# Kernel optimization log

Hardware: AMD Instinct MI355X
Metric: run time of the kernel (lower is better)

The kernel has to match this reference:

```python
import jax, jax.numpy as jnp
import numpy as np

N_QUBITS = 4
NOISE_RATE = 0.01  # depolarizing channel scales Pauli-Z expectation by (1 - p)


def _rx_mat(theta):
    # RX(theta) = [[cos(t/2), -i sin(t/2)], [-i sin(t/2), cos(t/2)]]; theta scalar or (b,)
    c = jnp.cos(theta / 2).astype(jnp.complex64)
    s = (-1j * jnp.sin(theta / 2)).astype(jnp.complex64)
    return jnp.stack([jnp.stack([c, s], -1), jnp.stack([s, c], -1)], -2)


def _apply_1q(state, mat, wire):
    # state: (b, 2,2,2,2); mat: (2,2) shared or (b,2,2) per-sample
    st = jnp.moveaxis(state, wire + 1, -1)
    if mat.ndim == 2:
        st = st @ mat.T
    else:
        st = jnp.einsum('b...j,bij->b...i', st, mat)
    return jnp.moveaxis(st, -1, wire + 1)


def _cnot(state, src, tgt):
    st = jnp.moveaxis(state, (src + 1, tgt + 1), (-2, -1))
    st = jnp.concatenate([st[..., 0:1, :], st[..., 1:2, ::-1]], axis=-2)
    return jnp.moveaxis(st, (-2, -1), (src + 1, tgt + 1))


def _qlayer(x, theta):
    # x: (b, n_qubits) encoding angles; theta: (n_params,) trainable RX angles
    b = x.shape[0]
    state = jnp.zeros((b,) + (2,) * N_QUBITS, jnp.complex64)
    state = state.at[(slice(None),) + (0,) * N_QUBITS].set(1.0)
    for w in range(N_QUBITS):                      # GeneralEncoder: RX(x_w) on wire w
        state = _apply_1q(state, _rx_mat(x[:, w]), w)
    for k in range(theta.shape[0]):                # trainable RX_k on wire k
        state = _apply_1q(state, _rx_mat(theta[k]), k)
    for i in range(N_QUBITS):                      # CNOT ring (i, (i+1)%n)
        state = _cnot(state, i, (i + 1) % N_QUBITS)
    p = jnp.abs(state) ** 2                        # (b, 2,2,2,2)
    ez = []
    for w in range(N_QUBITS):                      # <Z_w> = P(0) - P(1)
        axes = tuple(a for a in range(1, N_QUBITS + 1) if a != w + 1)
        m = p.sum(axes)
        ez.append(m[:, 0] - m[:, 1])
    return (1.0 - NOISE_RATE) * jnp.stack(ez, -1)  # depolarizing noise on expectations


def reference(inputs, w_lin, b_lin, w_map, b_map, theta):
    # inputs: (S, B, D); gate order: forget, input, update, output
    S, B, D = inputs.shape
    H = w_map.shape[1]
    hx0 = jnp.zeros((B, H), inputs.dtype)
    cx0 = jnp.zeros((B, H), inputs.dtype)
    qbatch = jax.vmap(_qlayer)  # over the 4 gates

    def step(carry, x):
        hx, cx = carry
        comb = jnp.concatenate([x, hx], axis=1)                      # (B, D+H)
        pre = jnp.einsum('gqd,bd->gbq', w_lin, comb) + b_lin[:, None, :]
        q = qbatch(pre, theta)                                       # (4, B, n_qubits)
        acts = jnp.stack([jax.nn.sigmoid(q[0]), jax.nn.sigmoid(q[1]),
                          jnp.tanh(q[2]), jax.nn.sigmoid(q[3])])
        gates = jnp.einsum('ghq,gbq->gbh', w_map, acts) + b_map[:, None, :]
        f, i_, g, o = gates
        cx2 = f * cx + i_ * g
        hx2 = o * jnp.tanh(cx2)
        return (hx2, cx2), hx2

    (hx, cx), outputs = jax.lax.scan(step, (hx0, cx0), inputs)
    return outputs, hx, cx


def setup_inputs() -> dict:
    key = jax.random.key(0)
    ks = jax.random.split(key, 6)
    S, B, D, H, NQ, NG = 512, 256, 128, 256, 4, 4
    return {
        'inputs': jax.random.normal(ks[0], (S, B, D), jnp.float32),
        'w_lin': jax.random.normal(ks[1], (NG, NQ, D + H), jnp.float32) * 0.05,
        'b_lin': jax.random.normal(ks[2], (NG, NQ), jnp.float32) * 0.05,
        'w_map': jax.random.normal(ks[3], (NG, H, NQ), jnp.float32) * 0.3,
        'b_map': jax.random.normal(ks[4], (NG, H), jnp.float32) * 0.05,
        'theta': jax.random.uniform(ks[5], (NG, 4), jnp.float32, 0.0, 2.0 * np.pi),
    }
```

## Files before the change

kernel.cpp:

```cpp
#include <hip/hip_runtime.h>

#define SEQ   512
#define BATCH 256
#define DIN   128
#define HID   256
#define NOISE 0.99f

__device__ __forceinline__ float dot4(float4 a, float4 b) {
    return fmaf(a.x, b.x, fmaf(a.y, b.y, fmaf(a.z, b.z, a.w * b.w)));
}
__device__ __forceinline__ float sigmoid_(float x) {
    return __builtin_amdgcn_rcpf(1.0f + __expf(-x));
}
__device__ __forceinline__ float tanh_(float x) {
    float ax = fabsf(x);
    float e  = __expf(2.0f * ax);
    float t  = __builtin_amdgcn_rcpf(e + 1.0f);
    float r  = 1.0f - 2.0f * t;
    return copysignf(r, x);
}

template <int CTRL>
__device__ __forceinline__ float dppmov(float v) {
    return __int_as_float(__builtin_amdgcn_mov_dpp(__float_as_int(v), CTRL, 0xF, 0xF, false));
}
__device__ __forceinline__ float swap16_sum(float v) {
    float a = v, b;
    asm("v_mov_b32 %1, %0\n\tv_permlane16_swap_b32 %0, %1" : "+v"(a), "=&v"(b));
    return a + b;
}
__device__ __forceinline__ float swap32_sum(float v) {
    float a = v, b;
    asm("v_mov_b32 %1, %0\n\tv_permlane32_swap_b32 %0, %1" : "+v"(a), "=&v"(b));
    return a + b;
}

__device__ __forceinline__ void barrier_lds() {
    asm volatile("s_waitcnt lgkmcnt(0)\n\ts_barrier" ::: "memory");
}

__global__ __launch_bounds__(256, 4) void pre_gemm(
    const float* __restrict__ x,
    const float* __restrict__ w_lin,
    const float* __restrict__ b_lin,
    const float* __restrict__ theta,
    float* pre, int pstride)
{
    __shared__ float wlds[16 * 132];
    const int t = threadIdx.x;
    for (int i = t; i < 16 * 128; i += 256) {
        int pp = i >> 7, dd = i & 127;
        wlds[pp * 132 + dd] = w_lin[pp * 384 + dd];
    }
    __syncthreads();
    const int s = blockIdx.x >> 4;
    const int b = ((blockIdx.x & 15) << 4) + (t >> 4);
    const int p = t & 15;
    const float* xr = x + ((size_t)s * BATCH + b) * DIN;
    const float* wr = &wlds[p * 132];
    float acc = b_lin[p] + theta[p];
    #pragma unroll 8
    for (int d = 0; d < 32; ++d)
        acc += dot4(*(const float4*)(xr + d * 4), *(const float4*)(wr + d * 4));
    pre[((size_t)s * BATCH + b) * pstride + p] = acc;
}

__global__ __launch_bounds__(256, 1) void qlstm_rec(
    const float* __restrict__ w_lin,
    const float* __restrict__ w_map,
    const float* __restrict__ b_map,
    const float* pre, int pstride,
    float* out)
{
    const int b = blockIdx.x;
    const int t = threadIdx.x;
    const int l = t & 63;
    const int g = t >> 6;
    const int q = l & 3;
    const int j = l >> 2;
    const int p = (g << 2) | q;

    __shared__ __align__(16) float hx_lds[HID];
    __shared__ __align__(16) float acts_lds[16];

    const int sig = (j >> 1) & 3;
    const float* wp = w_lin + p * 384 + 128 + j * 16;
    const float4 wh0 = *(const float4*)(wp + ((0 ^ sig) << 2));
    const float4 wh1 = *(const float4*)(wp + ((1 ^ sig) << 2));
    const float4 wh2 = *(const float4*)(wp + ((2 ^ sig) << 2));
    const float4 wh3 = *(const float4*)(wp + ((3 ^ sig) << 2));

    const float4 wm0 = ((const float4*)w_map)[0 * 256 + t];
    const float4 wm1 = ((const float4*)w_map)[1 * 256 + t];
    const float4 wm2 = ((const float4*)w_map)[2 * 256 + t];
    const float4 wm3 = ((const float4*)w_map)[3 * 256 + t];
    const float bm0 = b_map[t];
    const float bm1 = b_map[256 + t];
    const float bm2 = b_map[512 + t];
    const float bm3 = b_map[768 + t];

    const float* hr = &hx_lds[j * 16];
    const float* hr0 = hr + ((0 ^ sig) << 2);
    const float* hr1 = hr + ((1 ^ sig) << 2);
    const float* hr2 = hr + ((2 ^ sig) << 2);
    const float* hr3 = hr + ((3 ^ sig) << 2);

    const float*  pb      = pre + (size_t)b * pstride + p;
    const size_t  sstride = (size_t)BATCH * pstride;
    float px0 = pb[0];
    float px1 = pb[sstride];

    hx_lds[t] = 0.0f;
    float hx = 0.0f, cx = 0.0f;
    float* out_seq = out;
    float* out_hx  = out + (size_t)SEQ * BATCH * HID;
    float* out_cx  = out_hx + BATCH * HID;
    barrier_lds();

    for (int s = 0; s < SEQ; ++s) {
        const float pxu = px0;
        px0 = px1;
        const int s2 = (s + 2 < SEQ) ? s + 2 : SEQ - 1;
        px1 = pb[(size_t)s2 * sstride];

        const float4 ha0 = *(const float4*)hr0;
        const float4 ha1 = *(const float4*)hr1;
        const float4 ha2 = *(const float4*)hr2;
        const float4 ha3 = *(const float4*)hr3;
        float acc = dot4(wh0, ha0) + dot4(wh1, ha1)
                  + dot4(wh2, ha2) + dot4(wh3, ha3);
        acc += dppmov<0x124>(acc);
        acc += dppmov<0x128>(acc);
        acc  = swap16_sum(acc);
        acc  = swap32_sum(acc);

        const float A  = __cosf(acc + pxu);
        const float Bv = dppmov<0xB1>(A);
        const float Cv = dppmov<0x4E>(A);
        const float Dv = dppmov<0x4E>(Bv);

        const float t1 = Cv * Dv;
        const float u  = (q & 1) ? (A * Bv) : ((q == 2) ? A : Bv);
        const float v  = (q == 1) ? 1.0f : t1;
        const float ez = NOISE * u * v;
        const float act = (g == 2) ? tanh_(ez) : sigmoid_(ez);
        if (l < 4) acts_lds[(g << 2) | l] = act;
        barrier_lds();

        const float4 a0 = *(const float4*)&acts_lds[0];
        const float4 a1 = *(const float4*)&acts_lds[4];
        const float4 a2 = *(const float4*)&acts_lds[8];
        const float4 a3 = *(const float4*)&acts_lds[12];

        const float fv = bm0 + dot4(wm0, a0);
        const float iv = bm1 + dot4(wm1, a1);
        const float gv = bm2 + dot4(wm2, a2);
        const float ov = bm3 + dot4(wm3, a3);

        cx = fmaf(fv, cx, iv * gv);
        hx = ov * tanh_(cx);

        hx_lds[t] = hx;
        out_seq[((size_t)s * BATCH + b) * HID + t] = hx;
        barrier_lds();
    }

    out_hx[(size_t)b * HID + t] = hx;
    out_cx[(size_t)b * HID + t] = cx;
}

extern "C" void kernel_launch(void* const* d_in, const int* in_sizes, int n_in,
                              void* d_out, int out_size, void* d_ws, size_t ws_size,
                              hipStream_t stream) {
    const float* x     = (const float*)d_in[0];
    const float* w_lin = (const float*)d_in[1];
    const float* b_lin = (const float*)d_in[2];
    const float* w_map = (const float*)d_in[3];
    const float* b_map = (const float*)d_in[4];
    const float* theta = (const float*)d_in[5];
    float* out = (float*)d_out;

    const size_t pre_bytes = (size_t)SEQ * BATCH * 16 * sizeof(float);
    float* pre;
    int pstride;
    if (ws_size >= pre_bytes) {
        pre = (float*)d_ws;
        pstride = 16;
    } else {
        pre = out;
        pstride = HID;
    }

    pre_gemm<<<dim3(SEQ * 16), dim3(256), 0, stream>>>(x, w_lin, b_lin, theta, pre, pstride);
    qlstm_rec<<<dim3(BATCH), dim3(256), 0, stream>>>(w_lin, w_map, b_map, pre, pstride, out);
}
```

Baseline: 273.9 us.

## Interleave two batch rows per block to overlap recurrent phases across barriers

Each block of the recurrent kernel now handles two batch rows. The update phase of one row runs alongside the quantum-layer phase of the other, so each barrier interval does useful work for both rows and the serial barrier-latency chain is spread over two independent recurrences. The grid shrinks to 128 blocks, which leaves half of the 256 CUs on the MI355X idle, and per-thread work and register use per interval go up.

```diff
diff --git a/kernel.cpp b/kernel.cpp
--- a/kernel.cpp
+++ b/kernel.cpp
@@ -19,7 +19,6 @@
     float r  = 1.0f - 2.0f * t;
     return copysignf(r, x);
 }
-
 template <int CTRL>
 __device__ __forceinline__ float dppmov(float v) {
     return __int_as_float(__builtin_amdgcn_mov_dpp(__float_as_int(v), CTRL, 0xF, 0xF, false));
@@ -34,7 +33,6 @@
     asm("v_mov_b32 %1, %0\n\tv_permlane32_swap_b32 %0, %1" : "+v"(a), "=&v"(b));
     return a + b;
 }
-
 __device__ __forceinline__ void barrier_lds() {
     asm volatile("s_waitcnt lgkmcnt(0)\n\ts_barrier" ::: "memory");
 }
@@ -72,7 +70,8 @@
     const float* pre, int pstride,
     float* out)
 {
-    const int b = blockIdx.x;
+    const int bA = blockIdx.x * 2;
+    const int bB = bA + 1;
     const int t = threadIdx.x;
     const int l = t & 63;
     const int g = t >> 6;
@@ -80,8 +79,10 @@
     const int j = l >> 2;
     const int p = (g << 2) | q;
 
-    __shared__ __align__(16) float hx_lds[HID];
-    __shared__ __align__(16) float acts_lds[16];
+    __shared__ __align__(16) float hxA_lds[HID];
+    __shared__ __align__(16) float hxB_lds[HID];
+    __shared__ __align__(16) float actsA_lds[16];
+    __shared__ __align__(16) float actsB_lds[16];
 
     const int sig = (j >> 1) & 3;
     const float* wp = w_lin + p * 384 + 128 + j * 16;
@@ -99,74 +100,117 @@
     const float bm2 = b_map[512 + t];
     const float bm3 = b_map[768 + t];
 
-    const float* hr = &hx_lds[j * 16];
-    const float* hr0 = hr + ((0 ^ sig) << 2);
-    const float* hr1 = hr + ((1 ^ sig) << 2);
-    const float* hr2 = hr + ((2 ^ sig) << 2);
-    const float* hr3 = hr + ((3 ^ sig) << 2);
-
-    const float*  pb      = pre + (size_t)b * pstride + p;
-    const size_t  sstride = (size_t)BATCH * pstride;
-    float px0 = pb[0];
-    float px1 = pb[sstride];
-
-    hx_lds[t] = 0.0f;
-    float hx = 0.0f, cx = 0.0f;
-    float* out_seq = out;
-    float* out_hx  = out + (size_t)SEQ * BATCH * HID;
-    float* out_cx  = out_hx + BATCH * HID;
-    barrier_lds();
-
-    for (int s = 0; s < SEQ; ++s) {
-        const float pxu = px0;
-        px0 = px1;
-        const int s2 = (s + 2 < SEQ) ? s + 2 : SEQ - 1;
-        px1 = pb[(size_t)s2 * sstride];
-
-        const float4 ha0 = *(const float4*)hr0;
-        const float4 ha1 = *(const float4*)hr1;
-        const float4 ha2 = *(const float4*)hr2;
-        const float4 ha3 = *(const float4*)hr3;
+    const int o0 = j * 16 + ((0 ^ sig) << 2);
+    const int o1 = j * 16 + ((1 ^ sig) << 2);
+    const int o2 = j * 16 + ((2 ^ sig) << 2);
+    const int o3 = j * 16 + ((3 ^ sig) << 2);
+
+    const size_t sstride = (size_t)BATCH * pstride;
+    const float* pbA = pre + (size_t)bA * pstride + p;
+    const float* pbB = pre + (size_t)bB * pstride + p;
+    float pxB0 = pbB[0];
+    float pxB1 = pbB[sstride];
+
+    hxA_lds[t] = 0.0f;
+    hxB_lds[t] = 0.0f;
+    float hxA = 0.0f, cxA = 0.0f, hxB = 0.0f, cxB = 0.0f;
+    float* out_hx = out + (size_t)SEQ * BATCH * HID;
+    float* out_cx = out_hx + BATCH * HID;
+
+    auto P1 = [&](float4 ha0, float4 ha1, float4 ha2, float4 ha3, float pxu) -> float {
         float acc = dot4(wh0, ha0) + dot4(wh1, ha1)
                   + dot4(wh2, ha2) + dot4(wh3, ha3);
         acc += dppmov<0x124>(acc);
         acc += dppmov<0x128>(acc);
         acc  = swap16_sum(acc);
         acc  = swap32_sum(acc);
-
         const float A  = __cosf(acc + pxu);
         const float Bv = dppmov<0xB1>(A);
         const float Cv = dppmov<0x4E>(A);
         const float Dv = dppmov<0x4E>(Bv);
-
         const float t1 = Cv * Dv;
         const float u  = (q & 1) ? (A * Bv) : ((q == 2) ? A : Bv);
         const float v  = (q == 1) ? 1.0f : t1;
         const float ez = NOISE * u * v;
-        const float act = (g == 2) ? tanh_(ez) : sigmoid_(ez);
-        if (l < 4) acts_lds[(g << 2) | l] = act;
-        barrier_lds();
-
-        const float4 a0 = *(const float4*)&acts_lds[0];
-        const float4 a1 = *(const float4*)&acts_lds[4];
-        const float4 a2 = *(const float4*)&acts_lds[8];
-        const float4 a3 = *(const float4*)&acts_lds[12];
-
+        return (g == 2) ? tanh_(ez) : sigmoid_(ez);
+    };
+    auto P2 = [&](float4 a0, float4 a1, float4 a2, float4 a3, float& cx, float& hx) {
         const float fv = bm0 + dot4(wm0, a0);
         const float iv = bm1 + dot4(wm1, a1);
         const float gv = bm2 + dot4(wm2, a2);
         const float ov = bm3 + dot4(wm3, a3);
-
         cx = fmaf(fv, cx, iv * gv);
         hx = ov * tanh_(cx);
-
-        hx_lds[t] = hx;
-        out_seq[((size_t)s * BATCH + b) * HID + t] = hx;
+    };
+
+    barrier_lds();
+
+    {
+        const float4 ha0 = *(const float4*)(hxA_lds + o0);
+        const float4 ha1 = *(const float4*)(hxA_lds + o1);
+        const float4 ha2 = *(const float4*)(hxA_lds + o2);
+        const float4 ha3 = *(const float4*)(hxA_lds + o3);
+        const float act = P1(ha0, ha1, ha2, ha3, pbA[0]);
+        if (l < 4) actsA_lds[(g << 2) | l] = act;
+    }
+    float pxA0 = pbA[sstride];
+    float pxA1 = pbA[2 * sstride];
+    barrier_lds();
+
+    for (int k = 0; k < SEQ; ++k) {
+        {
+            const float4 aA0 = *(const float4*)&actsA_lds[0];
+            const float4 aA1 = *(const float4*)&actsA_lds[4];
+            const float4 aA2 = *(const float4*)&actsA_lds[8];
+            const float4 aA3 = *(const float4*)&actsA_lds[12];
+            const float4 hB0 = *(const float4*)(hxB_lds + o0);
+            const float4 hB1 = *(const float4*)(hxB_lds + o1);
+            const float4 hB2 = *(const float4*)(hxB_lds + o2);
+            const float4 hB3 = *(const float4*)(hxB_lds + o3);
+
+            P2(aA0, aA1, aA2, aA3, cxA, hxA);
+
+            const float pxuB = pxB0;
+            pxB0 = pxB1;
+            const int sB2 = (k + 2 < SEQ) ? k + 2 : SEQ - 1;
+            pxB1 = pbB[(size_t)sB2 * sstride];
+            const float actB = P1(hB0, hB1, hB2, hB3, pxuB);
+
+            hxA_lds[t] = hxA;
+            out[((size_t)k * BATCH + bA) * HID + t] = hxA;
+            if (l < 4) actsB_lds[(g << 2) | l] = actB;
+        }
         barrier_lds();
-    }
-
-    out_hx[(size_t)b * HID + t] = hx;
-    out_cx[(size_t)b * HID + t] = cx;
+
+        {
+            const float4 hA0 = *(const float4*)(hxA_lds + o0);
+            const float4 hA1 = *(const float4*)(hxA_lds + o1);
+            const float4 hA2 = *(const float4*)(hxA_lds + o2);
+            const float4 hA3 = *(const float4*)(hxA_lds + o3);
+            const float4 aB0 = *(const float4*)&actsB_lds[0];
+            const float4 aB1 = *(const float4*)&actsB_lds[4];
+            const float4 aB2 = *(const float4*)&actsB_lds[8];
+            const float4 aB3 = *(const float4*)&actsB_lds[12];
+
+            P2(aB0, aB1, aB2, aB3, cxB, hxB);
+
+            const float pxuA = pxA0;
+            pxA0 = pxA1;
+            const int sA2 = (k + 3 < SEQ) ? k + 3 : SEQ - 1;
+            pxA1 = pbA[(size_t)sA2 * sstride];
+            const float actA = P1(hA0, hA1, hA2, hA3, pxuA);
+
+            hxB_lds[t] = hxB;
+            out[((size_t)k * BATCH + bB) * HID + t] = hxB;
+            if (l < 4) actsA_lds[(g << 2) | l] = actA;
+        }
+        barrier_lds();
+    }
+
+    out_hx[(size_t)bA * HID + t] = hxA;
+    out_cx[(size_t)bA * HID + t] = cxA;
+    out_hx[(size_t)bB * HID + t] = hxB;
+    out_cx[(size_t)bB * HID + t] = cxB;
 }
 
 extern "C" void kernel_launch(void* const* d_in, const int* in_sizes, int n_in,
@@ -192,5 +236,5 @@
     }
 
     pre_gemm<<<dim3(SEQ * 16), dim3(256), 0, stream>>>(x, w_lin, b_lin, theta, pre, pstride);
-    qlstm_rec<<<dim3(BATCH), dim3(256), 0, stream>>>(w_lin, w_map, b_map, pre, pstride, out);
-}
+    qlstm_rec<<<dim3(BATCH / 2), dim3(256), 0, stream>>>(w_lin, w_map, b_map, pre, pstride, out);
+}
```

Measured after the change: 412.2 us. +50.5%, slower.

## Compute gate mapping per wave before barrier using readlane activations

Applied to the files above, without the earlier changes.

Each wave now reads its gate's four activations with readlane and computes four hidden units' mapped gate values for that gate before the barrier, writing them to a 4x256 LDS array. After the barrier each thread reads its four gate values instead of loading 16 activations and doing four dot products. This moves the mapping work ahead of the barrier so it overlaps across waves instead of running after it, and shortens the post-barrier critical path. The cost is more LDS traffic per step (a float4 store and four scalar loads) and more scalar readlane instructions.

```diff
diff --git a/kernel.cpp b/kernel.cpp
--- a/kernel.cpp
+++ b/kernel.cpp
@@ -19,7 +19,6 @@
     float r  = 1.0f - 2.0f * t;
     return copysignf(r, x);
 }
-
 template <int CTRL>
 __device__ __forceinline__ float dppmov(float v) {
     return __int_as_float(__builtin_amdgcn_mov_dpp(__float_as_int(v), CTRL, 0xF, 0xF, false));
@@ -34,7 +33,9 @@
     asm("v_mov_b32 %1, %0\n\tv_permlane32_swap_b32 %0, %1" : "+v"(a), "=&v"(b));
     return a + b;
 }
-
+__device__ __forceinline__ float rdlanef(float v, int lane) {
+    return __int_as_float(__builtin_amdgcn_readlane(__float_as_int(v), lane));
+}
 __device__ __forceinline__ void barrier_lds() {
     asm volatile("s_waitcnt lgkmcnt(0)\n\ts_barrier" ::: "memory");
 }
@@ -81,7 +82,7 @@
     const int p = (g << 2) | q;
 
     __shared__ __align__(16) float hx_lds[HID];
-    __shared__ __align__(16) float acts_lds[16];
+    __shared__ __align__(16) float gates_lds[4][HID];
 
     const int sig = (j >> 1) & 3;
     const float* wp = w_lin + p * 384 + 128 + j * 16;
@@ -90,14 +91,11 @@
     const float4 wh2 = *(const float4*)(wp + ((2 ^ sig) << 2));
     const float4 wh3 = *(const float4*)(wp + ((3 ^ sig) << 2));
 
-    const float4 wm0 = ((const float4*)w_map)[0 * 256 + t];
-    const float4 wm1 = ((const float4*)w_map)[1 * 256 + t];
-    const float4 wm2 = ((const float4*)w_map)[2 * 256 + t];
-    const float4 wm3 = ((const float4*)w_map)[3 * 256 + t];
-    const float bm0 = b_map[t];
-    const float bm1 = b_map[256 + t];
-    const float bm2 = b_map[512 + t];
-    const float bm3 = b_map[768 + t];
+    const float4 wmg0 = ((const float4*)w_map)[g * 256 + 4 * l + 0];
+    const float4 wmg1 = ((const float4*)w_map)[g * 256 + 4 * l + 1];
+    const float4 wmg2 = ((const float4*)w_map)[g * 256 + 4 * l + 2];
+    const float4 wmg3 = ((const float4*)w_map)[g * 256 + 4 * l + 3];
+    const float4 bmg  = *(const float4*)(b_map + g * 256 + 4 * l);
 
     const float* hr = &hx_lds[j * 16];
     const float* hr0 = hr + ((0 ^ sig) << 2);
@@ -144,20 +142,24 @@
         const float v  = (q == 1) ? 1.0f : t1;
         const float ez = NOISE * u * v;
         const float act = (g == 2) ? tanh_(ez) : sigmoid_(ez);
-        if (l < 4) acts_lds[(g << 2) | l] = act;
+
+        const float4 av = make_float4(rdlanef(act, 0), rdlanef(act, 1),
+                                      rdlanef(act, 2), rdlanef(act, 3));
+
+        float4 gv4;
+        gv4.x = bmg.x + dot4(wmg0, av);
+        gv4.y = bmg.y + dot4(wmg1, av);
+        gv4.z = bmg.z + dot4(wmg2, av);
+        gv4.w = bmg.w + dot4(wmg3, av);
+        *(float4*)&gates_lds[g][4 * l] = gv4;
         barrier_lds();
 
-        const float4 a0 = *(const float4*)&acts_lds[0];
-        const float4 a1 = *(const float4*)&acts_lds[4];
-        const float4 a2 = *(const float4*)&acts_lds[8];
-        const float4 a3 = *(const float4*)&acts_lds[12];
+        const float fv = gates_lds[0][t];
+        const float iv = gates_lds[1][t];
+        const float gvv = gates_lds[2][t];
+        const float ov = gates_lds[3][t];
 
-        const float fv = bm0 + dot4(wm0, a0);
-        const float iv = bm1 + dot4(wm1, a1);
-        const float gv = bm2 + dot4(wm2, a2);
-        const float ov = bm3 + dot4(wm3, a3);
-
-        cx = fmaf(fv, cx, iv * gv);
+        cx = fmaf(fv, cx, iv * gvv);
         hx = ov * tanh_(cx);
 
         hx_lds[t] = hx;
```

After: 286.2 us. 1.04x slower.

## Fuse input projection GEMM into recurrent kernel via per-block LDS buffer

Applied to the files above, without the earlier changes.

Removes the separate pre_gemm launch and the global workspace round trip. Each recurrent block now computes its own batch row's input projections for all 512 timesteps into a 32 KB LDS buffer before the recurrence, then reads them from LDS each step. This saves a kernel launch and the global write/read of the pre-activations. In exchange, the projection work runs with only 256 blocks instead of 8192 and sits serially in front of the recurrence, with strided global reads of x per block.

```diff
diff --git a/kernel.cpp b/kernel.cpp
--- a/kernel.cpp
+++ b/kernel.cpp
@@ -19,7 +19,6 @@
     float r  = 1.0f - 2.0f * t;
     return copysignf(r, x);
 }
-
 template <int CTRL>
 __device__ __forceinline__ float dppmov(float v) {
     return __int_as_float(__builtin_amdgcn_mov_dpp(__float_as_int(v), CTRL, 0xF, 0xF, false));
@@ -34,54 +33,53 @@
     asm("v_mov_b32 %1, %0\n\tv_permlane32_swap_b32 %0, %1" : "+v"(a), "=&v"(b));
     return a + b;
 }
-
 __device__ __forceinline__ void barrier_lds() {
     asm volatile("s_waitcnt lgkmcnt(0)\n\ts_barrier" ::: "memory");
 }
 
-__global__ __launch_bounds__(256, 4) void pre_gemm(
+__global__ __launch_bounds__(256, 1) void qlstm_fused(
     const float* __restrict__ x,
     const float* __restrict__ w_lin,
     const float* __restrict__ b_lin,
+    const float* __restrict__ w_map,
+    const float* __restrict__ b_map,
     const float* __restrict__ theta,
-    float* pre, int pstride)
+    float* __restrict__ out)
 {
-    __shared__ float wlds[16 * 132];
+    const int b = blockIdx.x;
     const int t = threadIdx.x;
+
+    __shared__ __align__(16) float pre_lds[SEQ * 16];
+    __shared__ __align__(16) float wlds[16 * 132];
+    __shared__ __align__(16) float hx_lds[HID];
+    __shared__ __align__(16) float acts_lds[16];
+
     for (int i = t; i < 16 * 128; i += 256) {
         int pp = i >> 7, dd = i & 127;
         wlds[pp * 132 + dd] = w_lin[pp * 384 + dd];
     }
-    __syncthreads();
-    const int s = blockIdx.x >> 4;
-    const int b = ((blockIdx.x & 15) << 4) + (t >> 4);
-    const int p = t & 15;
-    const float* xr = x + ((size_t)s * BATCH + b) * DIN;
-    const float* wr = &wlds[p * 132];
-    float acc = b_lin[p] + theta[p];
-    #pragma unroll 8
-    for (int d = 0; d < 32; ++d)
-        acc += dot4(*(const float4*)(xr + d * 4), *(const float4*)(wr + d * 4));
-    pre[((size_t)s * BATCH + b) * pstride + p] = acc;
-}
+    barrier_lds();
+    {
+        const int sp = t >> 4;
+        const int pp = t & 15;
+        const float* wr = &wlds[pp * 132];
+        const float bt = b_lin[pp] + theta[pp];
+        for (int i = 0; i < 32; ++i) {
+            const int s = i * 16 + sp;
+            const float* xr = x + ((size_t)s * BATCH + b) * DIN;
+            float acc = bt;
+            #pragma unroll 8
+            for (int d = 0; d < 32; ++d)
+                acc += dot4(*(const float4*)(xr + d * 4), *(const float4*)(wr + d * 4));
+            pre_lds[s * 16 + pp] = acc;
+        }
+    }
 
-__global__ __launch_bounds__(256, 1) void qlstm_rec(
-    const float* __restrict__ w_lin,
-    const float* __restrict__ w_map,
-    const float* __restrict__ b_map,
-    const float* pre, int pstride,
-    float* out)
-{
-    const int b = blockIdx.x;
-    const int t = threadIdx.x;
     const int l = t & 63;
     const int g = t >> 6;
     const int q = l & 3;
     const int j = l >> 2;
     const int p = (g << 2) | q;
-
-    __shared__ __align__(16) float hx_lds[HID];
-    __shared__ __align__(16) float acts_lds[16];
 
     const int sig = (j >> 1) & 3;
     const float* wp = w_lin + p * 384 + 128 + j * 16;
@@ -105,11 +103,6 @@
     const float* hr2 = hr + ((2 ^ sig) << 2);
     const float* hr3 = hr + ((3 ^ sig) << 2);
 
-    const float*  pb      = pre + (size_t)b * pstride + p;
-    const size_t  sstride = (size_t)BATCH * pstride;
-    float px0 = pb[0];
-    float px1 = pb[sstride];
-
     hx_lds[t] = 0.0f;
     float hx = 0.0f, cx = 0.0f;
     float* out_seq = out;
@@ -117,11 +110,12 @@
     float* out_cx  = out_hx + BATCH * HID;
     barrier_lds();
 
+    float px0 = pre_lds[p];
+
     for (int s = 0; s < SEQ; ++s) {
         const float pxu = px0;
-        px0 = px1;
-        const int s2 = (s + 2 < SEQ) ? s + 2 : SEQ - 1;
-        px1 = pb[(size_t)s2 * sstride];
+        const int s1 = (s + 1 < SEQ) ? s + 1 : SEQ - 1;
+        px0 = pre_lds[s1 * 16 + p];
 
         const float4 ha0 = *(const float4*)hr0;
         const float4 ha1 = *(const float4*)hr1;
@@ -180,17 +174,6 @@
     const float* theta = (const float*)d_in[5];
     float* out = (float*)d_out;
 
-    const size_t pre_bytes = (size_t)SEQ * BATCH * 16 * sizeof(float);
-    float* pre;
-    int pstride;
-    if (ws_size >= pre_bytes) {
-        pre = (float*)d_ws;
-        pstride = 16;
-    } else {
-        pre = out;
-        pstride = HID;
-    }
-
-    pre_gemm<<<dim3(SEQ * 16), dim3(256), 0, stream>>>(x, w_lin, b_lin, theta, pre, pstride);
-    qlstm_rec<<<dim3(BATCH), dim3(256), 0, stream>>>(w_lin, w_map, b_map, pre, pstride, out);
+    qlstm_fused<<<dim3(BATCH), dim3(256), 0, stream>>>(
+        x, w_lin, b_lin, w_map, b_map, theta, out);
 }
```

Result: no change. 268.8 us (-1.9%).
